# Kernel tuning notes

Measured on AMD Instinct MI355X. Metric: run time of the kernel, lower is better.

The kernel has to match this reference:

```python
import jax, jax.numpy as jnp
import numpy as np

N, E, NREL = 50000, 800000, 4
IN, EMB, HID, OUT, LVL = 32, 32, 32, 32, 3


def setup_inputs() -> dict:
    key = jax.random.key(0)
    ks = jax.random.split(key, 24)
    f32 = jnp.float32
    inp = {
        'x': jax.random.normal(ks[0], (N, IN), f32),
        'node_feat': jax.random.normal(ks[1], (N, EMB), f32),
        'edge_feat': jax.random.normal(ks[2], (E, EMB), f32),
        'src': jax.random.randint(ks[3], (E,), 0, N, jnp.int32),
        'dst': jax.random.randint(ks[4], (E,), 0, N, jnp.int32),
        'eid': jax.random.randint(ks[5], (E,), 0, NREL, jnp.int32),
        # layer 1 (in_feat=IN)
        'Wr1': jax.random.normal(ks[6], (NREL, IN + 2 * EMB, HID), f32) * 0.1,
        'attn_w1': jax.random.normal(ks[7], (EMB + HID, 1), f32) * 0.1,
        'loop_w1': jax.random.normal(ks[8], (EMB, HID), f32) * 0.1,
        'h_bias1': jax.random.normal(ks[9], (HID,), f32) * 0.1,
        'amrm_W1': jax.random.normal(ks[10], (LVL, HID, HID), f32) * 0.1,
        'amrm_b1': jax.random.normal(ks[11], (LVL, HID), f32) * 0.1,
        'amrm_a1': jax.random.normal(ks[12], (HID, 1), f32) * 0.1,
        # layer 2 (in_feat=HID)
        'Wr2': jax.random.normal(ks[13], (NREL, HID + 2 * EMB, OUT), f32) * 0.1,
        'attn_w2': jax.random.normal(ks[14], (EMB + OUT, 1), f32) * 0.1,
        'loop_w2': jax.random.normal(ks[15], (EMB, OUT), f32) * 0.1,
        'h_bias2': jax.random.normal(ks[16], (OUT,), f32) * 0.1,
        'amrm_W2': jax.random.normal(ks[17], (LVL, OUT, OUT), f32) * 0.1,
        'amrm_b2': jax.random.normal(ks[18], (LVL, OUT), f32) * 0.1,
        'amrm_a2': jax.random.normal(ks[19], (OUT, 1), f32) * 0.1,
    }
    return inp


def _rp_layer(feat, node_feat, src, dst, eid, edge_feat,
              Wr, attn_w, loop_w, h_bias, amrm_W, amrm_b, amrm_a):
    n = node_feat.shape[0]
    ones_e = jnp.ones((src.shape[0],), feat.dtype)
    # symmetric-ish degree norm: feat scaled by out-degree^-1/2
    deg_out = jnp.clip(jax.ops.segment_sum(ones_e, src, num_segments=n), 1.0)
    feat = feat * (deg_out ** -0.5)[:, None]
    # per-edge gather + relation-typed linear (grouped GEMM over NREL types)
    xe = jnp.concatenate([feat[src], edge_feat, node_feat[dst]], axis=1)  # [E, in+2*emb]
    m = jnp.zeros((xe.shape[0], Wr.shape[2]), feat.dtype)
    for r in range(Wr.shape[0]):
        m = m + jnp.where((eid == r)[:, None], xe @ Wr[r], 0.0)
    # edge attention + segment softmax over incoming edges per dst node
    z = jax.nn.leaky_relu(jnp.concatenate([node_feat[dst], m], axis=1) @ attn_w)  # [E,1]
    zmax = jax.ops.segment_max(z, dst, num_segments=n)
    ez = jnp.exp(z - zmax[dst])
    a = ez / jax.ops.segment_sum(ez, dst, num_segments=n)[dst]
    # scatter-sum aggregation
    h = jax.ops.segment_sum(a * m, dst, num_segments=n)
    h = h + node_feat @ loop_w
    deg_in = jnp.clip(jax.ops.segment_sum(ones_e, dst, num_segments=n), 1.0)
    h = h * (deg_in ** -0.5)[:, None] + h_bias
    # adaptive multi-level relation module
    lv = jax.nn.relu(jnp.einsum('nh,lho->nlo', h, amrm_W) + amrm_b[None])  # [N,L,O]
    sc = jax.nn.softmax(jnp.einsum('nlo,o->nl', lv, amrm_a[:, 0]), axis=-1)  # [N,L]
    return jnp.einsum('nl,nlo->no', sc, lv)


def reference(x, node_feat, edge_feat, src, dst, eid,
              Wr1, attn_w1, loop_w1, h_bias1, amrm_W1, amrm_b1, amrm_a1,
              Wr2, attn_w2, loop_w2, h_bias2, amrm_W2, amrm_b2, amrm_a2):
    h = jax.nn.relu(_rp_layer(x, node_feat, src, dst, eid, edge_feat,
                              Wr1, attn_w1, loop_w1, h_bias1, amrm_W1, amrm_b1, amrm_a1))
    h = jax.nn.relu(_rp_layer(h, node_feat, src, dst, eid, edge_feat,
                              Wr2, attn_w2, loop_w2, h_bias2, amrm_W2, amrm_b2, amrm_a2))
    return h
```

## Files before the change

### kernel.cpp

```cpp
#include <hip/hip_runtime.h>

#define NN 50000
#define NE 800000

#define O_DEGIN   0
#define O_DEGOUT  50048
#define O_ROWPTR  100096
#define O_CURSOR  150208
#define O_EINFO   200256
#define O_FEATN   1800256
#define O_ZF      3400256
#define O_ZNRD    3600320
#define O_VV      3800384
#define O_EZ      3800832
#define O_NFT     4600832
#define O_WDENT   6200832
#define O_YACCT   6450880
#define O_H1      19250880


__global__ __launch_bounds__(256) void k_deg(const int* __restrict__ src,
                                             const int* __restrict__ dst,
                                             int* degin, int* degout) {
    int e = blockIdx.x * 256 + threadIdx.x;
    if (e < NE) {
        atomicAdd(&degin[dst[e]], 1);
        atomicAdd(&degout[src[e]], 1);
    }
}

__global__ __launch_bounds__(1024) void k_scan(const int* __restrict__ degin,
                                               int* rowptr, int* cursor) {
    __shared__ int swsum[16];
    __shared__ int stot;
    int t = threadIdx.x;
    int lane = t & 63, w = t >> 6;
    int carry = 0;
    for (int ch = 0; ch < 4; ch++) {
        int base = ch * 16384 + t * 16;
        int v[16];
        int s = 0;
#pragma unroll
        for (int j = 0; j < 16; j++) {
            v[j] = (base + j < NN) ? degin[base + j] : 0;
            s += v[j];
        }
        int incl = s;
#pragma unroll
        for (int off = 1; off < 64; off <<= 1) {
            int x = __shfl_up(incl, off, 64);
            if (lane >= off) incl += x;
        }
        if (lane == 63) swsum[w] = incl;
        __syncthreads();
        if (w == 0) {
            int y = (lane < 16) ? swsum[lane] : 0;
            int yi = y;
#pragma unroll
            for (int off = 1; off < 16; off <<= 1) {
                int x = __shfl_up(yi, off, 64);
                if (lane >= off) yi += x;
            }
            if (lane < 16) swsum[lane] = yi - y;
            if (lane == 15) stot = yi;
        }
        __syncthreads();
        int excl = carry + swsum[w] + (incl - s);
#pragma unroll
        for (int j = 0; j < 16; j++) {
            if (base + j < NN) { rowptr[base + j] = excl; cursor[base + j] = excl; }
            excl += v[j];
        }
        carry += stot;
        __syncthreads();
    }
    if (t == 0) rowptr[NN] = carry;
}

__global__ __launch_bounds__(256) void k_scatter(const int* __restrict__ src,
                                                 const int* __restrict__ dst,
                                                 const int* __restrict__ eid,
                                                 int* cursor, int2* einfo) {
    int e = blockIdx.x * 256 + threadIdx.x;
    if (e >= NE) return;
    int slot = atomicAdd(&cursor[dst[e]], 1);
    einfo[slot] = make_int2(src[e] | (eid[e] << 20), e);
}


__global__ __launch_bounds__(384) void k_prevec(const float* __restrict__ Wr,
                                                const float* __restrict__ attw,
                                                float* __restrict__ vvec) {
    int t = threadIdx.x;
    int r = (t >> 5) & 3, k = t & 31, part = t >> 7;
    int row = (part == 0) ? (32 + k) : (part == 1) ? k : (64 + k);
    const float* wrow = Wr + (size_t)r * 3072 + row * 32;
    float s = 0.f;
#pragma unroll
    for (int c = 0; c < 32; c++) s += wrow[c] * attw[32 + c];
    vvec[t] = s;
}

__global__ __launch_bounds__(128) void k_nodeproj(const float* __restrict__ feat,
                                                  const float* __restrict__ nfeat,
                                                  const float* __restrict__ attw,
                                                  const float* __restrict__ vvec,
                                                  const int* __restrict__ degout,
                                                  float* __restrict__ featn,
                                                  float* __restrict__ nfT,
                                                  float* __restrict__ zF,
                                                  float* __restrict__ znrd) {
    int n = blockIdx.x * 128 + threadIdx.x;
    if (n >= NN) return;
    int dg = degout[n];
    float sc0 = rsqrtf((float)(dg > 1 ? dg : 1));
    const float* fin = feat + (size_t)n * 32;
    const float* nin = nfeat + (size_t)n * 32;
    float fv[32], nv[32];
#pragma unroll
    for (int k = 0; k < 32; k += 4) {
        float4 f4 = *(const float4*)&fin[k];
        fv[k] = f4.x * sc0; fv[k + 1] = f4.y * sc0;
        fv[k + 2] = f4.z * sc0; fv[k + 3] = f4.w * sc0;
        float4 n4 = *(const float4*)&nin[k];
        nv[k] = n4.x; nv[k + 1] = n4.y; nv[k + 2] = n4.z; nv[k + 3] = n4.w;
    }
    float* fo = featn + (size_t)n * 32;
#pragma unroll
    for (int k = 0; k < 32; k += 4)
        *(float4*)&fo[k] = make_float4(fv[k], fv[k + 1], fv[k + 2], fv[k + 3]);
#pragma unroll
    for (int k = 0; k < 32; k++) nfT[(size_t)k * NN + n] = nv[k];
    float zn = 0.f;
#pragma unroll
    for (int k = 0; k < 32; k++) zn += nv[k] * attw[k];
#pragma unroll
    for (int r = 0; r < 4; r++) {
        float zf = 0.f, zd = 0.f;
        const float* vf = vvec + 128 + r * 32;
        const float* vd = vvec + 256 + r * 32;
#pragma unroll
        for (int k = 0; k < 32; k++) { zf += fv[k] * vf[k]; zd += nv[k] * vd[k]; }
        zF[r * NN + n] = zf;
        znrd[r * NN + n] = zn + zd;
    }
}

__global__ __launch_bounds__(256) void k_ez(const int* __restrict__ src,
                                            const int* __restrict__ dst,
                                            const int* __restrict__ eid,
                                            const float* __restrict__ efeat,
                                            const float* __restrict__ zF,
                                            const float* __restrict__ znrd,
                                            const float* __restrict__ vvec,
                                            float* __restrict__ ez) {
    int e = blockIdx.x * 256 + threadIdx.x;
    int s = src[e], d = dst[e], r = eid[e];
    const float* er = efeat + (size_t)e * 32;
    float d0 = 0.f, d1 = 0.f, d2 = 0.f, d3 = 0.f;
#pragma unroll
    for (int k = 0; k < 32; k += 4) {
        float4 f = *(const float4*)&er[k];
        d0 += f.x * vvec[k]       + f.y * vvec[k + 1]
            + f.z * vvec[k + 2]   + f.w * vvec[k + 3];
        d1 += f.x * vvec[32 + k]  + f.y * vvec[33 + k]
            + f.z * vvec[34 + k]  + f.w * vvec[35 + k];
        d2 += f.x * vvec[64 + k]  + f.y * vvec[65 + k]
            + f.z * vvec[66 + k]  + f.w * vvec[67 + k];
        d3 += f.x * vvec[96 + k]  + f.y * vvec[97 + k]
            + f.z * vvec[98 + k]  + f.w * vvec[99 + k];
    }
    float dot = (r == 0) ? d0 : (r == 1) ? d1 : (r == 2) ? d2 : d3;
    float z = znrd[r * NN + d] + zF[r * NN + s] + dot;
    z = z > 0.f ? z : 0.01f * z;
    ez[e] = __expf(z);
}

__global__ __launch_bounds__(512) void k_agg(const int* __restrict__ rowptr,
                                             const int2* __restrict__ einfo,
                                             const float* __restrict__ ez,
                                             const float* __restrict__ efeat,
                                             const float* __restrict__ featn,
                                             float* __restrict__ yaccT,
                                             float* __restrict__ wdenT) {
    __shared__ float sT[256 * 9];
    int tid = threadIdx.x;
    int lane = tid & 63;
    int wid = tid >> 6;
    int n0 = blockIdx.x * 8;
    int n = n0 + wid;
    int c = lane & 31;
    int p = lane >> 5;

    int rp0 = rowptr[n];
    int deg = rowptr[n + 1] - rp0;

    float yf0 = 0.f, yf1 = 0.f, yf2 = 0.f, yf3 = 0.f;
    float ye0 = 0.f, ye1 = 0.f, ye2 = 0.f, ye3 = 0.f;
    float w0 = 0.f, w1 = 0.f, w2 = 0.f, w3 = 0.f, den = 0.f;

    int2 meA = make_int2(0, 0), meB = make_int2(0, 0);
    float ezA = 0.f, efA = 0.f, fnA = 0.f;
    if (p < deg) {
        meA = einfo[rp0 + p];
        ezA = ez[meA.y];
        efA = efeat[(size_t)meA.y * 32 + c];
        fnA = featn[(size_t)(meA.x & 0xFFFFF) * 32 + c];
    }
    if (p + 2 < deg) meB = einfo[rp0 + p + 2];

    for (int t = p; t < deg; t += 2) {
        float ezB = 0.f, efB = 0.f, fnB = 0.f;
        int2 meC = make_int2(0, 0);
        if (t + 2 < deg) {
            ezB = ez[meB.y];
            efB = efeat[(size_t)meB.y * 32 + c];
            fnB = featn[(size_t)(meB.x & 0xFFFFF) * 32 + c];
        }
        if (t + 4 < deg) meC = einfo[rp0 + t + 4];
        int rb = meA.x >> 20;
        float e0 = (rb == 0) ? ezA : 0.f;
        float e1 = (rb == 1) ? ezA : 0.f;
        float e2 = (rb == 2) ? ezA : 0.f;
        float e3 = (rb == 3) ? ezA : 0.f;
        yf0 += e0 * fnA; yf1 += e1 * fnA; yf2 += e2 * fnA; yf3 += e3 * fnA;
        ye0 += e0 * efA; ye1 += e1 * efA; ye2 += e2 * efA; ye3 += e3 * efA;
        w0 += e0; w1 += e1; w2 += e2; w3 += e3;
        den += ezA;
        meA = meB; ezA = ezB; efA = efB; fnA = fnB; meB = meC;
    }

    yf0 += __shfl_xor(yf0, 32); yf1 += __shfl_xor(yf1, 32);
    yf2 += __shfl_xor(yf2, 32); yf3 += __shfl_xor(yf3, 32);
    ye0 += __shfl_xor(ye0, 32); ye1 += __shfl_xor(ye1, 32);
    ye2 += __shfl_xor(ye2, 32); ye3 += __shfl_xor(ye3, 32);
    w0 += __shfl_xor(w0, 32); w1 += __shfl_xor(w1, 32);
    w2 += __shfl_xor(w2, 32); w3 += __shfl_xor(w3, 32);
    den += __shfl_xor(den, 32);

    if (lane < 5) {
        float wv = (lane == 0) ? w0 : (lane == 1) ? w1 : (lane == 2) ? w2
                 : (lane == 3) ? w3 : den;
        wdenT[lane * NN + n] = wv;
    }

    {
        int kb = 128 * p + c;
        sT[(kb +  0) * 9 + wid] = p ? ye0 : yf0;
        sT[(kb + 32) * 9 + wid] = p ? ye1 : yf1;
        sT[(kb + 64) * 9 + wid] = p ? ye2 : yf2;
        sT[(kb + 96) * 9 + wid] = p ? ye3 : yf3;
    }
    __syncthreads();
    int k = tid >> 1, hf = tid & 1;
    float4 v = make_float4(sT[k * 9 + hf * 4 + 0], sT[k * 9 + hf * 4 + 1],
                           sT[k * 9 + hf * 4 + 2], sT[k * 9 + hf * 4 + 3]);
    *(float4*)&yaccT[(size_t)k * NN + n0 + hf * 4] = v;
}

__global__ __launch_bounds__(256) void k_postAB(const int* __restrict__ rowptr,
                                                const float* __restrict__ yaccT,
                                                const float* __restrict__ wdenT,
                                                const float* __restrict__ nfT,
                                                const float* __restrict__ Wr,
                                                const float* __restrict__ lw,
                                                const float* __restrict__ hbias,
                                                const float* __restrict__ aW,
                                                const float* __restrict__ ab,
                                                const float* __restrict__ aa,
                                                float* __restrict__ out) {
    int n = blockIdx.x * 256 + threadIdx.x;
    if (n >= NN) return;
    int deg = rowptr[n + 1] - rowptr[n];
    float den = wdenT[(size_t)4 * NN + n];
    float invden = (deg > 0) ? 1.f / den : 0.f;

    float nv[32];
#pragma unroll
    for (int k = 0; k < 32; k++) nv[k] = nfT[(size_t)k * NN + n];

    float acc[32];
#pragma unroll
    for (int i = 0; i < 32; i++) acc[i] = 0.f;

#pragma unroll 1
    for (int r = 0; r < 4; r++) {
        float wr = wdenT[(size_t)r * NN + n];
        const float* W = Wr + (size_t)r * 3072;
        const float* ufc = yaccT + (size_t)(r * 32) * NN + n;
        const float* uec = yaccT + (size_t)(128 + r * 32) * NN + n;
        for (int k4 = 0; k4 < 32; k4 += 4) {
            float a0 = ufc[(size_t)(k4 + 0) * NN], a1 = ufc[(size_t)(k4 + 1) * NN];
            float a2 = ufc[(size_t)(k4 + 2) * NN], a3 = ufc[(size_t)(k4 + 3) * NN];
            float b0 = uec[(size_t)(k4 + 0) * NN], b1 = uec[(size_t)(k4 + 1) * NN];
            float b2 = uec[(size_t)(k4 + 2) * NN], b3 = uec[(size_t)(k4 + 3) * NN];
            float g0 = wr * nv[k4],     g1 = wr * nv[k4 + 1];
            float g2 = wr * nv[k4 + 2], g3 = wr * nv[k4 + 3];
            const float* Wk = W + k4 * 32;
#pragma unroll
            for (int i = 0; i < 32; i++)
                acc[i] += a0 * Wk[i]        + a1 * Wk[32 + i]
                        + a2 * Wk[64 + i]   + a3 * Wk[96 + i]
                        + b0 * Wk[1024 + i] + b1 * Wk[1056 + i]
                        + b2 * Wk[1088 + i] + b3 * Wk[1120 + i]
                        + g0 * Wk[2048 + i] + g1 * Wk[2080 + i]
                        + g2 * Wk[2112 + i] + g3 * Wk[2144 + i];
        }
    }

    float h[32];
#pragma unroll
    for (int i = 0; i < 32; i++) h[i] = acc[i] * invden;
    for (int k4 = 0; k4 < 32; k4 += 4) {
        const float* Lk = lw + k4 * 32;
#pragma unroll
        for (int i = 0; i < 32; i++)
            h[i] += nv[k4] * Lk[i] + nv[k4 + 1] * Lk[32 + i]
                  + nv[k4 + 2] * Lk[64 + i] + nv[k4 + 3] * Lk[96 + i];
    }
    float hsc = rsqrtf((float)(deg > 1 ? deg : 1));
#pragma unroll
    for (int i = 0; i < 32; i++) h[i] = h[i] * hsc + hbias[i];

    float s[3];
#pragma unroll 1
    for (int l = 0; l < 3; l++) {
        const float* A = aW + (size_t)l * 1024;
#pragma unroll
        for (int i = 0; i < 32; i++) acc[i] = ab[l * 32 + i];
        for (int k4 = 0; k4 < 32; k4 += 4) {
            const float* Ak = A + k4 * 32;
#pragma unroll
            for (int i = 0; i < 32; i++)
                acc[i] += h[k4] * Ak[i] + h[k4 + 1] * Ak[32 + i]
                        + h[k4 + 2] * Ak[64 + i] + h[k4 + 3] * Ak[96 + i];
        }
        float sl = 0.f;
#pragma unroll
        for (int i = 0; i < 32; i++) {
            float lv = acc[i] > 0.f ? acc[i] : 0.f;
            sl += lv * aa[i];
        }
        s[l] = sl;
    }
    float mx = fmaxf(s[0], fmaxf(s[1], s[2]));
    float e0 = __expf(s[0] - mx), e1 = __expf(s[1] - mx), e2 = __expf(s[2] - mx);
    float inv = 1.f / (e0 + e1 + e2);
    float scl[3] = {e0 * inv, e1 * inv, e2 * inv};

    float outv[32];
#pragma unroll
    for (int i = 0; i < 32; i++) outv[i] = 0.f;
#pragma unroll 1
    for (int l = 0; l < 3; l++) {
        const float* A = aW + (size_t)l * 1024;
#pragma unroll
        for (int i = 0; i < 32; i++) acc[i] = ab[l * 32 + i];
        for (int k4 = 0; k4 < 32; k4 += 4) {
            const float* Ak = A + k4 * 32;
#pragma unroll
            for (int i = 0; i < 32; i++)
                acc[i] += h[k4] * Ak[i] + h[k4 + 1] * Ak[32 + i]
                        + h[k4 + 2] * Ak[64 + i] + h[k4 + 3] * Ak[96 + i];
        }
#pragma unroll
        for (int i = 0; i < 32; i++) {
            float lv = acc[i] > 0.f ? acc[i] : 0.f;
            outv[i] += scl[l] * lv;
        }
    }
    float* op = out + (size_t)n * 32;
#pragma unroll
    for (int i = 0; i < 32; i += 4)
        *(float4*)&op[i] = make_float4(fmaxf(outv[i], 0.f), fmaxf(outv[i + 1], 0.f),
                                       fmaxf(outv[i + 2], 0.f), fmaxf(outv[i + 3], 0.f));
}


static void launch_layer(const float* feat, const float* nf, const float* efeat,
                         const int* src, const int* dst, const int* eid,
                         const float* Wr, const float* attw, const float* lw,
                         const float* hb, const float* aW, const float* ab,
                         const float* aa, float* wsf, int* wsi, float* out,
                         hipStream_t stream) {
    k_prevec<<<1, 384, 0, stream>>>(Wr, attw, wsf + O_VV);
    k_nodeproj<<<391, 128, 0, stream>>>(feat, nf, attw, wsf + O_VV, wsi + O_DEGOUT,
                                        wsf + O_FEATN, wsf + O_NFT,
                                        wsf + O_ZF, wsf + O_ZNRD);
    k_ez<<<3125, 256, 0, stream>>>(src, dst, eid, efeat, wsf + O_ZF, wsf + O_ZNRD,
                                   wsf + O_VV, wsf + O_EZ);
    k_agg<<<6250, 512, 0, stream>>>(wsi + O_ROWPTR, (const int2*)(wsi + O_EINFO),
                                    wsf + O_EZ, efeat, wsf + O_FEATN,
                                    wsf + O_YACCT, wsf + O_WDENT);
    k_postAB<<<196, 256, 0, stream>>>(wsi + O_ROWPTR, wsf + O_YACCT, wsf + O_WDENT,
                                      wsf + O_NFT, Wr, lw, hb, aW, ab, aa, out);
}

extern "C" void kernel_launch(void* const* d_in, const int* in_sizes, int n_in,
                              void* d_out, int out_size, void* d_ws, size_t ws_size,
                              hipStream_t stream) {
    const float* x     = (const float*)d_in[0];
    const float* nfeat = (const float*)d_in[1];
    const float* efeat = (const float*)d_in[2];
    const int*   src   = (const int*)d_in[3];
    const int*   dst   = (const int*)d_in[4];
    const int*   eid   = (const int*)d_in[5];
    const float* Wr1   = (const float*)d_in[6];
    const float* attw1 = (const float*)d_in[7];
    const float* lw1   = (const float*)d_in[8];
    const float* hb1   = (const float*)d_in[9];
    const float* aW1   = (const float*)d_in[10];
    const float* ab1   = (const float*)d_in[11];
    const float* aa1   = (const float*)d_in[12];
    const float* Wr2   = (const float*)d_in[13];
    const float* attw2 = (const float*)d_in[14];
    const float* lw2   = (const float*)d_in[15];
    const float* hb2   = (const float*)d_in[16];
    const float* aW2   = (const float*)d_in[17];
    const float* ab2   = (const float*)d_in[18];
    const float* aa2   = (const float*)d_in[19];

    float* wsf = (float*)d_ws;
    int*   wsi = (int*)d_ws;
    float* out = (float*)d_out;

    hipMemsetAsync(d_ws, 0, (size_t)O_ROWPTR * 4, stream);

    k_deg<<<NE / 256, 256, 0, stream>>>(src, dst, wsi + O_DEGIN, wsi + O_DEGOUT);
    k_scan<<<1, 1024, 0, stream>>>(wsi + O_DEGIN, wsi + O_ROWPTR, wsi + O_CURSOR);
    k_scatter<<<NE / 256, 256, 0, stream>>>(src, dst, eid, wsi + O_CURSOR,
                                            (int2*)(wsi + O_EINFO));

    launch_layer(x, nfeat, efeat, src, dst, eid, Wr1, attw1, lw1, hb1, aW1, ab1, aa1,
                 wsf, wsi, wsf + O_H1, stream);
    launch_layer(wsf + O_H1, nfeat, efeat, src, dst, eid, Wr2, attw2, lw2, hb2,
                 aW2, ab2, aa2, wsf, wsi, out, stream);
}
```

Baseline: 816.2 us.

## Precompute per-relation node projections before aggregation to shrink post-aggregation GEMMs

Moves the feat·Wr_src, node_feat·Wr_dst and node_feat·loop_w projections into the per-node projection kernel, so aggregation gathers pre-projected per-relation source features and accumulates a single weighted sum instead of four relation-split ones. The post kernel then needs only the edge-feature GEMM plus cheap weighted combinations, and the aggregation kernel writes fewer transposed rows. In exchange the node kernel does much more FMA work per thread with heavy register pressure, and the gathered source table grows fourfold (128 floats per node), which raises the random-gather footprint during aggregation.

```diff
diff --git a/kernel.cpp b/kernel.cpp
--- a/kernel.cpp
+++ b/kernel.cpp
@@ -8,15 +8,16 @@
 #define O_ROWPTR  100096
 #define O_CURSOR  150208
 #define O_EINFO   200256
-#define O_FEATN   1800256
-#define O_ZF      3400256
-#define O_ZNRD    3600320
-#define O_VV      3800384
-#define O_EZ      3800832
-#define O_NFT     4600832
-#define O_WDENT   6200832
-#define O_YACCT   6450880
-#define O_H1      19250880
+#define O_FN2     1800256
+#define O_ZF      8200256
+#define O_ZNRD    8400256
+#define O_VV      8600256
+#define O_EZ      8600704
+#define O_NDT     9400704
+#define O_NLWT    15800704
+#define O_WDENT   17400704
+#define O_YT      17650704
+#define O_H1      25650704
 
 
 __global__ __launch_bounds__(256) void k_deg(const int* __restrict__ src,
@@ -106,8 +107,11 @@
                                                   const float* __restrict__ attw,
                                                   const float* __restrict__ vvec,
                                                   const int* __restrict__ degout,
-                                                  float* __restrict__ featn,
-                                                  float* __restrict__ nfT,
+                                                  const float* __restrict__ Wr,
+                                                  const float* __restrict__ lw,
+                                                  float* __restrict__ fn2,
+                                                  float* __restrict__ ndT,
+                                                  float* __restrict__ nlwT,
                                                   float* __restrict__ zF,
                                                   float* __restrict__ znrd) {
     int n = blockIdx.x * 128 + threadIdx.x;
@@ -125,12 +129,6 @@
         float4 n4 = *(const float4*)&nin[k];
         nv[k] = n4.x; nv[k + 1] = n4.y; nv[k + 2] = n4.z; nv[k + 3] = n4.w;
     }
-    float* fo = featn + (size_t)n * 32;
-#pragma unroll
-    for (int k = 0; k < 32; k += 4)
-        *(float4*)&fo[k] = make_float4(fv[k], fv[k + 1], fv[k + 2], fv[k + 3]);
-#pragma unroll
-    for (int k = 0; k < 32; k++) nfT[(size_t)k * NN + n] = nv[k];
     float zn = 0.f;
 #pragma unroll
     for (int k = 0; k < 32; k++) zn += nv[k] * attw[k];
@@ -143,6 +141,53 @@
         for (int k = 0; k < 32; k++) { zf += fv[k] * vf[k]; zd += nv[k] * vd[k]; }
         zF[r * NN + n] = zf;
         znrd[r * NN + n] = zn + zd;
+    }
+
+    float acc[32];
+#pragma unroll 1
+    for (int r = 0; r < 4; r++) {
+        const float* W = Wr + (size_t)r * 3072;
+#pragma unroll
+        for (int i = 0; i < 32; i++) acc[i] = 0.f;
+        for (int k4 = 0; k4 < 32; k4 += 4) {
+            const float* Wk = W + k4 * 32;
+#pragma unroll
+            for (int i = 0; i < 32; i++)
+                acc[i] += fv[k4] * Wk[i] + fv[k4 + 1] * Wk[32 + i]
+                        + fv[k4 + 2] * Wk[64 + i] + fv[k4 + 3] * Wk[96 + i];
+        }
+        float* fo = fn2 + (size_t)n * 128 + r * 32;
+#pragma unroll
+        for (int i = 0; i < 32; i += 4)
+            *(float4*)&fo[i] = make_float4(acc[i], acc[i + 1], acc[i + 2], acc[i + 3]);
+    }
+#pragma unroll 1
+    for (int r = 0; r < 4; r++) {
+        const float* W = Wr + (size_t)r * 3072 + 2048;
+#pragma unroll
+        for (int i = 0; i < 32; i++) acc[i] = 0.f;
+        for (int k4 = 0; k4 < 32; k4 += 4) {
+            const float* Wk = W + k4 * 32;
+#pragma unroll
+            for (int i = 0; i < 32; i++)
+                acc[i] += nv[k4] * Wk[i] + nv[k4 + 1] * Wk[32 + i]
+                        + nv[k4 + 2] * Wk[64 + i] + nv[k4 + 3] * Wk[96 + i];
+        }
+#pragma unroll
+        for (int i = 0; i < 32; i++) ndT[(size_t)(r * 32 + i) * NN + n] = acc[i];
+    }
+    {
+#pragma unroll
+        for (int i = 0; i < 32; i++) acc[i] = 0.f;
+        for (int k4 = 0; k4 < 32; k4 += 4) {
+            const float* Lk = lw + k4 * 32;
+#pragma unroll
+            for (int i = 0; i < 32; i++)
+                acc[i] += nv[k4] * Lk[i] + nv[k4 + 1] * Lk[32 + i]
+                        + nv[k4 + 2] * Lk[64 + i] + nv[k4 + 3] * Lk[96 + i];
+        }
+#pragma unroll
+        for (int i = 0; i < 32; i++) nlwT[(size_t)i * NN + n] = acc[i];
     }
 }
 
@@ -180,10 +225,10 @@
                                              const int2* __restrict__ einfo,
                                              const float* __restrict__ ez,
                                              const float* __restrict__ efeat,
-                                             const float* __restrict__ featn,
-                                             float* __restrict__ yaccT,
+                                             const float* __restrict__ fn2,
+                                             float* __restrict__ yT,
                                              float* __restrict__ wdenT) {
-    __shared__ float sT[256 * 9];
+    __shared__ float sT[160 * 9];
     int tid = threadIdx.x;
     int lane = tid & 63;
     int wid = tid >> 6;
@@ -195,7 +240,7 @@
     int rp0 = rowptr[n];
     int deg = rowptr[n + 1] - rp0;
 
-    float yf0 = 0.f, yf1 = 0.f, yf2 = 0.f, yf3 = 0.f;
+    float y = 0.f;
     float ye0 = 0.f, ye1 = 0.f, ye2 = 0.f, ye3 = 0.f;
     float w0 = 0.f, w1 = 0.f, w2 = 0.f, w3 = 0.f, den = 0.f;
 
@@ -205,7 +250,7 @@
         meA = einfo[rp0 + p];
         ezA = ez[meA.y];
         efA = efeat[(size_t)meA.y * 32 + c];
-        fnA = featn[(size_t)(meA.x & 0xFFFFF) * 32 + c];
+        fnA = fn2[(size_t)(meA.x & 0xFFFFF) * 128 + ((meA.x >> 20) << 5) + c];
     }
     if (p + 2 < deg) meB = einfo[rp0 + p + 2];
 
@@ -215,7 +260,7 @@
         if (t + 2 < deg) {
             ezB = ez[meB.y];
             efB = efeat[(size_t)meB.y * 32 + c];
-            fnB = featn[(size_t)(meB.x & 0xFFFFF) * 32 + c];
+            fnB = fn2[(size_t)(meB.x & 0xFFFFF) * 128 + ((meB.x >> 20) << 5) + c];
         }
         if (t + 4 < deg) meC = einfo[rp0 + t + 4];
         int rb = meA.x >> 20;
@@ -223,15 +268,14 @@
         float e1 = (rb == 1) ? ezA : 0.f;
         float e2 = (rb == 2) ? ezA : 0.f;
         float e3 = (rb == 3) ? ezA : 0.f;
-        yf0 += e0 * fnA; yf1 += e1 * fnA; yf2 += e2 * fnA; yf3 += e3 * fnA;
+        y += ezA * fnA;
         ye0 += e0 * efA; ye1 += e1 * efA; ye2 += e2 * efA; ye3 += e3 * efA;
         w0 += e0; w1 += e1; w2 += e2; w3 += e3;
         den += ezA;
         meA = meB; ezA = ezB; efA = efB; fnA = fnB; meB = meC;
     }
 
-    yf0 += __shfl_xor(yf0, 32); yf1 += __shfl_xor(yf1, 32);
-    yf2 += __shfl_xor(yf2, 32); yf3 += __shfl_xor(yf3, 32);
+    y += __shfl_xor(y, 32);
     ye0 += __shfl_xor(ye0, 32); ye1 += __shfl_xor(ye1, 32);
     ye2 += __shfl_xor(ye2, 32); ye3 += __shfl_xor(ye3, 32);
     w0 += __shfl_xor(w0, 32); w1 += __shfl_xor(w1, 32);
@@ -244,84 +288,74 @@
         wdenT[lane * NN + n] = wv;
     }
 
-    {
-        int kb = 128 * p + c;
-        sT[(kb +  0) * 9 + wid] = p ? ye0 : yf0;
-        sT[(kb + 32) * 9 + wid] = p ? ye1 : yf1;
-        sT[(kb + 64) * 9 + wid] = p ? ye2 : yf2;
-        sT[(kb + 96) * 9 + wid] = p ? ye3 : yf3;
+    if (p == 0) {
+        sT[(c +  0) * 9 + wid] = y;
+        sT[(c + 32) * 9 + wid] = ye0;
+        sT[(c + 64) * 9 + wid] = ye1;
+    } else {
+        sT[(c +  96) * 9 + wid] = ye2;
+        sT[(c + 128) * 9 + wid] = ye3;
     }
     __syncthreads();
-    int k = tid >> 1, hf = tid & 1;
-    float4 v = make_float4(sT[k * 9 + hf * 4 + 0], sT[k * 9 + hf * 4 + 1],
-                           sT[k * 9 + hf * 4 + 2], sT[k * 9 + hf * 4 + 3]);
-    *(float4*)&yaccT[(size_t)k * NN + n0 + hf * 4] = v;
-}
-
-__global__ __launch_bounds__(256) void k_postAB(const int* __restrict__ rowptr,
-                                                const float* __restrict__ yaccT,
-                                                const float* __restrict__ wdenT,
-                                                const float* __restrict__ nfT,
-                                                const float* __restrict__ Wr,
-                                                const float* __restrict__ lw,
-                                                const float* __restrict__ hbias,
-                                                const float* __restrict__ aW,
-                                                const float* __restrict__ ab,
-                                                const float* __restrict__ aa,
-                                                float* __restrict__ out) {
+    if (tid < 320) {
+        int k = tid >> 1, hf = tid & 1;
+        float4 v = make_float4(sT[k * 9 + hf * 4 + 0], sT[k * 9 + hf * 4 + 1],
+                               sT[k * 9 + hf * 4 + 2], sT[k * 9 + hf * 4 + 3]);
+        *(float4*)&yT[(size_t)k * NN + n0 + hf * 4] = v;
+    }
+}
+
+__global__ __launch_bounds__(256) void k_postB(const int* __restrict__ rowptr,
+                                               const float* __restrict__ yT,
+                                               const float* __restrict__ wdenT,
+                                               const float* __restrict__ ndT,
+                                               const float* __restrict__ nlwT,
+                                               const float* __restrict__ Wr,
+                                               const float* __restrict__ hbias,
+                                               const float* __restrict__ aW,
+                                               const float* __restrict__ ab,
+                                               const float* __restrict__ aa,
+                                               float* __restrict__ out) {
     int n = blockIdx.x * 256 + threadIdx.x;
     if (n >= NN) return;
     int deg = rowptr[n + 1] - rowptr[n];
     float den = wdenT[(size_t)4 * NN + n];
     float invden = (deg > 0) ? 1.f / den : 0.f;
 
-    float nv[32];
-#pragma unroll
-    for (int k = 0; k < 32; k++) nv[k] = nfT[(size_t)k * NN + n];
-
-    float acc[32];
-#pragma unroll
-    for (int i = 0; i < 32; i++) acc[i] = 0.f;
-
+    float h[32];
+#pragma unroll
+    for (int i = 0; i < 32; i++) h[i] = yT[(size_t)i * NN + n];
+
+#pragma unroll 1
+    for (int r = 0; r < 4; r++) {
+        float ye[32];
+#pragma unroll
+        for (int k = 0; k < 32; k++)
+            ye[k] = yT[(size_t)(32 + r * 32 + k) * NN + n];
+        const float* W = Wr + (size_t)r * 3072 + 1024;
+        for (int k4 = 0; k4 < 32; k4 += 4) {
+            const float* Wk = W + k4 * 32;
+#pragma unroll
+            for (int i = 0; i < 32; i++)
+                h[i] += ye[k4] * Wk[i] + ye[k4 + 1] * Wk[32 + i]
+                      + ye[k4 + 2] * Wk[64 + i] + ye[k4 + 3] * Wk[96 + i];
+        }
+    }
 #pragma unroll 1
     for (int r = 0; r < 4; r++) {
         float wr = wdenT[(size_t)r * NN + n];
-        const float* W = Wr + (size_t)r * 3072;
-        const float* ufc = yaccT + (size_t)(r * 32) * NN + n;
-        const float* uec = yaccT + (size_t)(128 + r * 32) * NN + n;
-        for (int k4 = 0; k4 < 32; k4 += 4) {
-            float a0 = ufc[(size_t)(k4 + 0) * NN], a1 = ufc[(size_t)(k4 + 1) * NN];
-            float a2 = ufc[(size_t)(k4 + 2) * NN], a3 = ufc[(size_t)(k4 + 3) * NN];
-            float b0 = uec[(size_t)(k4 + 0) * NN], b1 = uec[(size_t)(k4 + 1) * NN];
-            float b2 = uec[(size_t)(k4 + 2) * NN], b3 = uec[(size_t)(k4 + 3) * NN];
-            float g0 = wr * nv[k4],     g1 = wr * nv[k4 + 1];
-            float g2 = wr * nv[k4 + 2], g3 = wr * nv[k4 + 3];
-            const float* Wk = W + k4 * 32;
-#pragma unroll
-            for (int i = 0; i < 32; i++)
-                acc[i] += a0 * Wk[i]        + a1 * Wk[32 + i]
-                        + a2 * Wk[64 + i]   + a3 * Wk[96 + i]
-                        + b0 * Wk[1024 + i] + b1 * Wk[1056 + i]
-                        + b2 * Wk[1088 + i] + b3 * Wk[1120 + i]
-                        + g0 * Wk[2048 + i] + g1 * Wk[2080 + i]
-                        + g2 * Wk[2112 + i] + g3 * Wk[2144 + i];
-        }
-    }
-
-    float h[32];
-#pragma unroll
-    for (int i = 0; i < 32; i++) h[i] = acc[i] * invden;
-    for (int k4 = 0; k4 < 32; k4 += 4) {
-        const float* Lk = lw + k4 * 32;
 #pragma unroll
         for (int i = 0; i < 32; i++)
-            h[i] += nv[k4] * Lk[i] + nv[k4 + 1] * Lk[32 + i]
-                  + nv[k4 + 2] * Lk[64 + i] + nv[k4 + 3] * Lk[96 + i];
-    }
+            h[i] += wr * ndT[(size_t)(r * 32 + i) * NN + n];
+    }
+#pragma unroll
+    for (int i = 0; i < 32; i++)
+        h[i] = h[i] * invden + nlwT[(size_t)i * NN + n];
     float hsc = rsqrtf((float)(deg > 1 ? deg : 1));
 #pragma unroll
     for (int i = 0; i < 32; i++) h[i] = h[i] * hsc + hbias[i];
 
+    float acc[32];
     float s[3];
 #pragma unroll 1
     for (int l = 0; l < 3; l++) {
@@ -385,15 +419,16 @@
                          hipStream_t stream) {
     k_prevec<<<1, 384, 0, stream>>>(Wr, attw, wsf + O_VV);
     k_nodeproj<<<391, 128, 0, stream>>>(feat, nf, attw, wsf + O_VV, wsi + O_DEGOUT,
-                                        wsf + O_FEATN, wsf + O_NFT,
-                                        wsf + O_ZF, wsf + O_ZNRD);
+                                        Wr, lw, wsf + O_FN2, wsf + O_NDT,
+                                        wsf + O_NLWT, wsf + O_ZF, wsf + O_ZNRD);
     k_ez<<<3125, 256, 0, stream>>>(src, dst, eid, efeat, wsf + O_ZF, wsf + O_ZNRD,
                                    wsf + O_VV, wsf + O_EZ);
     k_agg<<<6250, 512, 0, stream>>>(wsi + O_ROWPTR, (const int2*)(wsi + O_EINFO),
-                                    wsf + O_EZ, efeat, wsf + O_FEATN,
-                                    wsf + O_YACCT, wsf + O_WDENT);
-    k_postAB<<<196, 256, 0, stream>>>(wsi + O_ROWPTR, wsf + O_YACCT, wsf + O_WDENT,
-                                      wsf + O_NFT, Wr, lw, hb, aW, ab, aa, out);
+                                    wsf + O_EZ, efeat, wsf + O_FN2,
+                                    wsf + O_YT, wsf + O_WDENT);
+    k_postB<<<196, 256, 0, stream>>>(wsi + O_ROWPTR, wsf + O_YT, wsf + O_WDENT,
+                                     wsf + O_NDT, wsf + O_NLWT, Wr, hb, aW, ab, aa,
+                                     out);
 }
 
 extern "C" void kernel_launch(void* const* d_in, const int* in_sizes, int n_in,
```

Result: faster. 780.2 us (-4.4%).
